# Kernel tuning notes

Measured on AMD Instinct MI355X. Metric: run time of the kernel, lower is better.

The kernel has to match this reference:

```python
import jax, jax.numpy as jnp
import numpy as np

B, N, DIM = 4, 4096, 512
HEADS, DIM_HEAD = 8, 64
DIM_INNER = HEADS * DIM_HEAD


def setup_inputs() -> dict:
    key = jax.random.key(0)
    k1, k2, k3 = jax.random.split(key, 3)
    x = jax.random.normal(k1, (B, N, DIM), dtype=jnp.float32)
    mask = jax.random.bernoulli(k2, 0.9, (B, N))
    W_qkv = jax.random.normal(k3, (DIM, 3 * DIM_INNER), dtype=jnp.float32) * (1.0 / np.sqrt(DIM))
    b_qkv = jnp.zeros((3 * DIM_INNER,), dtype=jnp.float32)
    return {"x": x, "mask": mask, "W_qkv": W_qkv, "b_qkv": b_qkv}


def reference(x, mask, W_qkv, b_qkv):
    # qkv projection: [b, n, 3*h*d]
    qkv = jnp.einsum('bnc,ce->bne', x, W_qkv) + b_qkv
    q, k, v = jnp.split(qkv, 3, axis=-1)

    def to_heads(t):  # b n (h d) -> b h n d
        b, n, _ = t.shape
        return t.reshape(b, n, HEADS, DIM_HEAD).transpose(0, 2, 1, 3)

    q, k, v = map(to_heads, (q, k, v))

    m = mask[:, None, :, None]  # b 1 n 1
    neg_max = -jnp.finfo(q.dtype).max
    k = jnp.where(m, k, neg_max)
    v = jnp.where(m, v, 0.0)

    k = jax.nn.softmax(k, axis=-2)  # softmax over sequence
    q = jax.nn.softmax(q, axis=-1)  # softmax over feature dim

    kv = jnp.einsum('bhnd,bhne->bhde', k, v)   # [b, h, d, d]
    out = jnp.einsum('bhde,bhnd->bhne', kv, q)  # [b, h, n, d]
    b_, h_, n_, d_ = out.shape
    return out.transpose(0, 2, 1, 3).reshape(b_, n_, h_ * d_)
```

## Files before the change

### kernel.cpp

```cpp
#include <hip/hip_runtime.h>
#include <stdint.h>

#define B_   4
#define N_   4096
#define DIM_ 512
#define H_   8
#define DH_  64
#define E3_  1536
#define M_   (B_*N_)

typedef __attribute__((ext_vector_type(8))) __bf16 bf16x8;
typedef __attribute__((ext_vector_type(8))) unsigned short ushort8;
typedef __attribute__((ext_vector_type(4))) float f32x4;

__device__ inline float bf2f(unsigned short u){ return __uint_as_float(((unsigned)u)<<16); }
__device__ inline unsigned short f2bf(float f){
  unsigned u = __float_as_uint(f);
  u += 0x7FFFu + ((u>>16)&1u);
  return (unsigned short)(u>>16);
}

__device__ inline void gld_lds16(const void* g, void* l){
  __builtin_amdgcn_global_load_lds(
      (const __attribute__((address_space(1))) void*)g,
      (__attribute__((address_space(3))) void*)l, 16, 0, 0);
}

__global__ void detect_fmt(const unsigned int* __restrict__ xw,
                           const unsigned int* __restrict__ ww,
                           const unsigned int* __restrict__ mw,
                           int* __restrict__ flags)
{
  __shared__ int cnt[2];
  __shared__ int ok[3];
  if (threadIdx.x < 2) cnt[threadIdx.x] = 0;
  if (threadIdx.x < 3) ok[threadIdx.x] = 1;
  __syncthreads();
  int hx = 0, hw = 0;
  for (int i = threadIdx.x; i < 1024; i += 256) {
    if (((xw[i] >> 7) & 0xFFu) > 140u) hx++;
    if (((ww[i] >> 7) & 0xFFu) > 140u) hw++;
  }
  int okInt = 1, okF32 = 1, okBf = 1;
  for (int i = threadIdx.x; i < 4096; i += 256) {
    unsigned w = mw[i];
    if (w > 1u) okInt = 0;
    if (w != 0u && w != 0x3F800000u) okF32 = 0;
    unsigned short a = (unsigned short)(w & 0xFFFFu), b = (unsigned short)(w >> 16);
    if (!((a == 0 || a == 0x3F80u) && (b == 0 || b == 0x3F80u))) okBf = 0;
  }
  atomicAdd(&cnt[0], hx);
  atomicAdd(&cnt[1], hw);
  if (!okInt) atomicAnd(&ok[0], 0);
  if (!okF32) atomicAnd(&ok[1], 0);
  if (!okBf)  atomicAnd(&ok[2], 0);
  __syncthreads();
  if (threadIdx.x == 0) {
    flags[0] = cnt[0] > 64 ? 1 : 0;
    flags[1] = cnt[1] > 64 ? 1 : 0;
    flags[2] = ok[0] ? 0 : (ok[1] ? 1 : (ok[2] ? 2 : 3));
  }
}

__device__ inline bool mask_at(const void* m, int flag, int idx){
  if (flag == 0) return ((const int*)m)[idx] != 0;
  if (flag == 1) return ((const float*)m)[idx] != 0.f;
  if (flag == 2) return ((const unsigned short*)m)[idx] != 0;
  return ((const unsigned char*)m)[idx] != 0;
}
__device__ inline float gread(const void* p, int f32, size_t i){
  return f32 ? ((const float*)p)[i] : bf2f(((const unsigned short*)p)[i]);
}

__global__ __launch_bounds__(256)
void pack_x(const void* __restrict__ x, unsigned short* __restrict__ xq,
            const int* __restrict__ flags)
{
  const int f = flags[0];
  const int g = blockIdx.x * 256 + threadIdx.x;
  const int R = g >> 13, rem = g & 8191;
  const int kk = rem >> 9, u = rem & 511;
  const int m = R * 128 + (u & 127);
  const int k0 = kk * 32 + (u >> 7) * 8;
  ushort8 v;
  if (f) {
    const float* xp = (const float*)x + (size_t)m * DIM_ + k0;
    float4 a = *(const float4*)xp, b = *(const float4*)(xp + 4);
    v[0]=f2bf(a.x); v[1]=f2bf(a.y); v[2]=f2bf(a.z); v[3]=f2bf(a.w);
    v[4]=f2bf(b.x); v[5]=f2bf(b.y); v[6]=f2bf(b.z); v[7]=f2bf(b.w);
  } else {
    v = *(const ushort8*)((const unsigned short*)x + (size_t)m * DIM_ + k0);
  }
  *(ushort8*)&xq[(size_t)g * 8] = v;
}

__global__ __launch_bounds__(256)
void pack_w(const void* __restrict__ w, unsigned short* __restrict__ wq,
            const int* __restrict__ flags)
{
  const int f = flags[1];
  const int g = blockIdx.x * 256 + threadIdx.x;
  const int C = g >> 13, rem = g & 8191;
  const int kk = rem >> 9, u = rem & 511;
  const int n = C * 128 + (u & 127);
  const int k0 = kk * 32 + (u >> 7) * 8;
  ushort8 v;
  #pragma unroll
  for (int j = 0; j < 8; ++j) v[j] = f2bf(gread(w, f, (size_t)(k0 + j) * E3_ + n));
  *(ushort8*)&wq[(size_t)g * 8] = v;
}

__global__ __launch_bounds__(256)
void qkv_gemm_fused(const unsigned short* __restrict__ xq,
                    const unsigned short* __restrict__ wq,
                    const void* __restrict__ bias, const void* __restrict__ mask,
                    const int* __restrict__ flags,
                    unsigned short* __restrict__ qb,
                    unsigned short* __restrict__ ekg,
                    unsigned short* __restrict__ vmg)
{
  const int wf = flags[1], mf = flags[2];
  __shared__ alignas(16) unsigned short As[512 * 8];
  __shared__ alignas(16) unsigned short Bs[512 * 8];
  const int t = threadIdx.x;
  const int lane = t & 63, wv = t >> 6;
  const int quad = lane >> 4, l15 = lane & 15;
  const int m0 = blockIdx.y * 128, n0 = blockIdx.x * 128;
  const int mw = (wv & 1) * 64, nw = (wv >> 1) * 64;

  f32x4 acc[4][4];
  #pragma unroll
  for (int i = 0; i < 4; ++i)
    #pragma unroll
    for (int j = 0; j < 4; ++j) acc[i][j] = (f32x4){0.f,0.f,0.f,0.f};

  for (int kk = 0; kk < 16; ++kk) {
    const unsigned short* aim = xq + ((size_t)(blockIdx.y * 16 + kk) * 512) * 8;
    const unsigned short* bim = wq + ((size_t)(blockIdx.x * 16 + kk) * 512) * 8;
    __syncthreads();
    #pragma unroll
    for (int s = 0; s < 2; ++s) {
      const int u0 = s * 256 + wv * 64;
      gld_lds16(aim + (size_t)(u0 + lane) * 8, &As[u0 * 8]);
      gld_lds16(bim + (size_t)(u0 + lane) * 8, &Bs[u0 * 8]);
    }
    __syncthreads();
    ushort8 af[4], bfr[4];
    #pragma unroll
    for (int i = 0; i < 4; ++i) {
      af[i]  = *(const ushort8*)&As[(quad * 128 + mw + i * 16 + l15) * 8];
      bfr[i] = *(const ushort8*)&Bs[(quad * 128 + nw + i * 16 + l15) * 8];
    }
    #pragma unroll
    for (int i = 0; i < 4; ++i)
      #pragma unroll
      for (int j = 0; j < 4; ++j)
        acc[i][j] = __builtin_amdgcn_mfma_f32_16x16x32_bf16(
            __builtin_bit_cast(bf16x8, af[i]), __builtin_bit_cast(bf16x8, bfr[j]),
            acc[i][j], 0, 0, 0);
  }

  const int mode = blockIdx.x >> 2;
  if (mode == 0) {
    #pragma unroll
    for (int j = 0; j < 4; ++j) {
      int col = n0 + nw + j * 16 + l15;
      float bv = gread(bias, wf, col);
      #pragma unroll
      for (int i = 0; i < 4; ++i)
        #pragma unroll
        for (int r = 0; r < 4; ++r) {
          int row = m0 + mw + i * 16 + quad * 4 + r;
          qb[(size_t)row * 512 + col] = f2bf(acc[i][j][r] + bv);
        }
    }
  } else {
    unsigned short* dstbuf = (mode == 1) ? ekg : vmg;
    float bj[4]; int hj[4], dj[4];
    #pragma unroll
    for (int j = 0; j < 4; ++j) {
      int col = n0 + nw + j * 16 + l15;
      bj[j] = gread(bias, wf, col);
      int rel = col - mode * 512;
      hj[j] = rel >> 6; dj[j] = rel & 63;
    }
    #pragma unroll
    for (int i = 0; i < 4; ++i)
      #pragma unroll
      for (int r = 0; r < 4; ++r) {
        int row = m0 + mw + i * 16 + quad * 4 + r;
        bool mk = mask_at(mask, mf, row);
        int b = row >> 12, nn = row & 4095;
        size_t base = (size_t)(nn >> 3) * 512 + (nn & 7);
        #pragma unroll
        for (int j = 0; j < 4; ++j) {
          float val = acc[i][j][r] + bj[j];
          val = (mode == 1) ? (mk ? __expf(val) : 0.f) : (mk ? val : 0.f);
          dstbuf[(size_t)(b * 8 + hj[j]) * 262144 + base + (size_t)dj[j] * 8] = f2bf(val);
        }
      }
  }
}

__global__ __launch_bounds__(256)
void kv_gemm(const unsigned short* __restrict__ ekg,
             const unsigned short* __restrict__ vmg,
             float* __restrict__ kvpart, float* __restrict__ denpart)
{
  const int kc8 = blockIdx.x;
  const int bh  = blockIdx.y;
  const int t   = threadIdx.x;
  const int lane = t & 63, wv = t >> 6;
  const int quad = lane >> 4, l15 = lane & 15;
  __shared__ alignas(16) unsigned short ekS[16384];
  __shared__ alignas(16) unsigned short vmS[16384];

  f32x4 acc[4];
  #pragma unroll
  for (int j = 0; j < 4; ++j) acc[j] = (f32x4){0.f,0.f,0.f,0.f};
  float dsum = 0.f;
  const int dden = t & 63, g0 = (t >> 6) * 8;

  for (int sc = 0; sc < 2; ++sc) {
    const size_t gbase = (size_t)bh * 262144 + (size_t)(kc8 * 2 + sc) * 16384;
    __syncthreads();
    #pragma unroll
    for (int i = 0; i < 8; ++i) {
      int u0 = i * 256 + wv * 64;
      gld_lds16(&ekg[gbase + (size_t)(u0 + lane) * 8], &ekS[u0 * 8]);
      gld_lds16(&vmg[gbase + (size_t)(u0 + lane) * 8], &vmS[u0 * 8]);
    }
    __syncthreads();
    {
      #pragma unroll
      for (int kt = 0; kt < 8; ++kt) {
        ushort8 v = *(const ushort8*)&ekS[((g0 + kt) * 64 + dden) * 8];
        #pragma unroll
        for (int j = 0; j < 8; ++j) dsum += bf2f(v[j]);
      }
    }
    #pragma unroll 2
    for (int ks = 0; ks < 8; ++ks) {
      ushort8 af = *(const ushort8*)&ekS[((ks * 4 + quad) * 64 + wv * 16 + l15) * 8];
      #pragma unroll
      for (int jt = 0; jt < 4; ++jt) {
        ushort8 bf8 = *(const ushort8*)&vmS[((ks * 4 + quad) * 64 + jt * 16 + l15) * 8];
        acc[jt] = __builtin_amdgcn_mfma_f32_16x16x32_bf16(
            __builtin_bit_cast(bf16x8, af), __builtin_bit_cast(bf16x8, bf8),
            acc[jt], 0, 0, 0);
      }
    }
  }
  float* kvp = kvpart + (size_t)(kc8 * 32 + bh) * 4096;
  #pragma unroll
  for (int jt = 0; jt < 4; ++jt)
    #pragma unroll
    for (int r = 0; r < 4; ++r)
      kvp[(wv * 16 + quad * 4 + r) * 64 + jt * 16 + l15] = acc[jt][r];
  __syncthreads();
  float* red = (float*)ekS;
  red[t] = dsum;
  __syncthreads();
  if (t < 64)
    denpart[(kc8 * 32 + bh) * 64 + t] = red[t] + red[t + 64] + red[t + 128] + red[t + 192];
}

__global__ __launch_bounds__(256)
void kv_reduce(const float* __restrict__ kvpart, const float* __restrict__ denpart,
               unsigned short* __restrict__ kvnb)
{
  const int bh = blockIdx.x;
  const int t  = threadIdx.x;
  __shared__ float den[64];
  if (t < 64) {
    float s = 0.f;
    #pragma unroll
    for (int c = 0; c < 8; ++c) s += denpart[(c * 32 + bh) * 64 + t];
    den[t] = s;
  }
  __syncthreads();
  const int d = t >> 2, e0 = (t & 3) * 16;
  const float inv = 1.f / den[d];
  #pragma unroll
  for (int j = 0; j < 16; ++j) {
    int e = e0 + j;
    float s = 0.f;
    #pragma unroll
    for (int c = 0; c < 8; ++c) s += kvpart[(size_t)(c * 32 + bh) * 4096 + d * 64 + e];
    kvnb[(size_t)bh * 4096 + ((size_t)(d >> 3) * 64 + e) * 8 + (d & 7)] = f2bf(s * inv);
  }
}

__global__ __launch_bounds__(256)
void out_pass(const unsigned short* __restrict__ qb,
              const unsigned short* __restrict__ kvnb,
              float* __restrict__ out)
{
  const int chunk = blockIdx.x, bh = blockIdx.y;
  const int b = bh >> 3, h = bh & 7;
  const int t = threadIdx.x;
  const int lane = t & 63, wv = t >> 6;
  const int quad = lane >> 4, l15 = lane & 15;
  __shared__ alignas(16) unsigned short kvS[4096];
  __shared__ alignas(16) unsigned short qsmb[1024];
  #pragma unroll
  for (int i = 0; i < 2; ++i)
    *(ushort8*)&kvS[(t + i * 256) * 8] =
        *(const ushort8*)&kvnb[(size_t)bh * 4096 + (size_t)(t + i * 256) * 8];

  const int tok = t >> 4, p = t & 15, d0 = p * 4;
  float qreg[4];
  {
    int row = b * N_ + chunk * 256 + tok;
    uint2 qw = *(const uint2*)(qb + (size_t)row * 512 + h * DH_ + d0);
    qreg[0] = bf2f((unsigned short)(qw.x & 0xffff));
    qreg[1] = bf2f((unsigned short)(qw.x >> 16));
    qreg[2] = bf2f((unsigned short)(qw.y & 0xffff));
    qreg[3] = bf2f((unsigned short)(qw.y >> 16));
  }
  for (int g = 0; g < 16; ++g) {
    const int row0 = b * N_ + chunk * 256 + g * 16;
    float mx = fmaxf(fmaxf(qreg[0], qreg[1]), fmaxf(qreg[2], qreg[3]));
    #pragma unroll
    for (int o = 1; o < 16; o <<= 1) mx = fmaxf(mx, __shfl_xor(mx, o, 16));
    float ex[4]; float s = 0.f;
    #pragma unroll
    for (int j = 0; j < 4; ++j) { ex[j] = __expf(qreg[j] - mx); s += ex[j]; }
    #pragma unroll
    for (int o = 1; o < 16; o <<= 1) s += __shfl_xor(s, o, 16);
    float inv = 1.f / s;
    __syncthreads();
    #pragma unroll
    for (int j = 0; j < 4; ++j)
      qsmb[((size_t)((d0 + j) >> 3) * 16 + tok) * 8 + ((d0 + j) & 7)] = f2bf(ex[j] * inv);
    if (g < 15) {
      uint2 qw = *(const uint2*)(qb + (size_t)(row0 + 16 + tok) * 512 + h * DH_ + d0);
      qreg[0] = bf2f((unsigned short)(qw.x & 0xffff));
      qreg[1] = bf2f((unsigned short)(qw.x >> 16));
      qreg[2] = bf2f((unsigned short)(qw.y & 0xffff));
      qreg[3] = bf2f((unsigned short)(qw.y >> 16));
    }
    __syncthreads();
    f32x4 acc = (f32x4){0.f,0.f,0.f,0.f};
    #pragma unroll
    for (int s2 = 0; s2 < 2; ++s2) {
      int koct = s2 * 4 + quad;
      ushort8 a8 = *(const ushort8*)&qsmb[(koct * 16 + l15) * 8];
      ushort8 b8 = *(const ushort8*)&kvS[(koct * 64 + wv * 16 + l15) * 8];
      acc = __builtin_amdgcn_mfma_f32_16x16x32_bf16(
          __builtin_bit_cast(bf16x8, a8), __builtin_bit_cast(bf16x8, b8), acc, 0, 0, 0);
    }
    #pragma unroll
    for (int r = 0; r < 4; ++r)
      out[(size_t)(row0 + quad * 4 + r) * 512 + h * DH_ + wv * 16 + l15] = acc[r];
  }
}

__device__ inline void stage_x_f(float (*xa)[516], const void* x, int xf, int brow0, int t)
{
  if (xf) {
    const float* xp = (const float*)x;
    #pragma unroll
    for (int s = 0; s < 8; ++s) {
      int row = (t >> 7) + 2 * s, col = (t & 127) * 4;
      *(float4*)&xa[row][col] = *(const float4*)(xp + ((size_t)(brow0 + row)) * DIM_ + col);
    }
  } else {
    const unsigned short* xp = (const unsigned short*)x;
    #pragma unroll
    for (int s = 0; s < 8; ++s) {
      int row = (t >> 7) + 2 * s, col = (t & 127) * 4;
      const unsigned short* pp = xp + ((size_t)(brow0 + row)) * DIM_ + col;
      #pragma unroll
      for (int j = 0; j < 4; ++j) xa[row][col + j] = bf2f(pp[j]);
    }
  }
}

__global__ __launch_bounds__(256)
void kv_pass_fused(const void* __restrict__ x, const void* __restrict__ w,
                   const void* __restrict__ bias, const void* __restrict__ mask,
                   const int* __restrict__ flags,
                   float* __restrict__ kvbuf, float* __restrict__ denom)
{
  const int chunk = blockIdx.x, bh = blockIdx.y;
  const int b = bh >> 3, h = bh & 7;
  const int t = threadIdx.x;
  const int xf = flags[0], wf = flags[1], mf = flags[2];
  __shared__ float xa[16][516];
  __shared__ float Wb[64][130];
  float* ekb = &Wb[0][0];
  float* vvb = &Wb[0][0] + 16 * 65;
  const int tok = t >> 4, d0 = (t & 15) * 4;
  const int down = t >> 2, e0 = (t & 3) * 16;
  float acc[16];
  #pragma unroll
  for (int i = 0; i < 16; ++i) acc[i] = 0.f;
  float dsum = 0.f;
  for (int g = 0; g < 16; ++g) {
    const int n0 = chunk * 256 + g * 16;
    __syncthreads();
    stage_x_f(xa, x, xf, b * N_ + n0, t);
    float kreg[4] = {0,0,0,0}, vreg[4] = {0,0,0,0};
    for (int cc = 0; cc < 8; ++cc) {
      __syncthreads();
      {
        int c0 = (t >> 7) * 32, col = t & 127;
        int wc = (col < 64) ? (512 + h * DH_ + col) : (1024 + h * DH_ + (col - 64));
        #pragma unroll 8
        for (int j = 0; j < 32; ++j)
          Wb[c0 + j][col] = gread(w, wf, (size_t)(cc * 64 + c0 + j) * E3_ + wc);
      }
      __syncthreads();
      #pragma unroll 4
      for (int c = 0; c < 64; ++c) {
        float xv = xa[tok][cc * 64 + c];
        #pragma unroll
        for (int j = 0; j < 4; ++j) {
          kreg[j] += xv * Wb[c][d0 + j];
          vreg[j] += xv * Wb[c][64 + d0 + j];
        }
      }
    }
    bool mk = mask_at(mask, mf, b * N_ + n0 + tok);
    __syncthreads();
    #pragma unroll
    for (int j = 0; j < 4; ++j) {
      float kvl = kreg[j] + gread(bias, wf, 512  + h * DH_ + d0 + j);
      float vvl = vreg[j] + gread(bias, wf, 1024 + h * DH_ + d0 + j);
      ekb[tok * 65 + d0 + j] = mk ? __expf(kvl) : 0.f;
      vvb[tok * 65 + d0 + j] = mk ? vvl : 0.f;
    }
    __syncthreads();
    #pragma unroll 4
    for (int nn = 0; nn < 16; ++nn) {
      float ekd = ekb[nn * 65 + down];
      if (e0 == 0) dsum += ekd;
      #pragma unroll
      for (int i = 0; i < 16; ++i) acc[i] += ekd * vvb[nn * 65 + e0 + i];
    }
  }
  float* kvp = kvbuf + (size_t)bh * 4096 + down * 64 + e0;
  #pragma unroll
  for (int i = 0; i < 16; ++i) atomicAdd(&kvp[i], acc[i]);
  if (e0 == 0) atomicAdd(&denom[bh * 64 + down], dsum);
}

__global__ __launch_bounds__(256)
void out_pass_fused(const void* __restrict__ x, const void* __restrict__ w,
                    const void* __restrict__ bias, const int* __restrict__ flags,
                    const float* __restrict__ kvbuf, const float* __restrict__ denom,
                    float* __restrict__ out)
{
  const int chunk = blockIdx.x, bh = blockIdx.y;
  const int b = bh >> 3, h = bh & 7;
  const int t = threadIdx.x;
  const int xf = flags[0], wf = flags[1];
  __shared__ float xa[16][516];
  __shared__ float Wq[64][66];
  __shared__ float kvn[64][68];
  float* qsm = &Wq[0][0];
  for (int i = t; i < 4096; i += 256) {
    int d = i >> 6, e = i & 63;
    kvn[d][e] = kvbuf[(size_t)bh * 4096 + i] / denom[bh * 64 + d];
  }
  const int tok = t >> 4, p = t & 15, d0 = p * 4;
  for (int g = 0; g < 16; ++g) {
    const int n0 = chunk * 256 + g * 16;
    __syncthreads();
    stage_x_f(xa, x, xf, b * N_ + n0, t);
    float qreg[4] = {0,0,0,0};
    for (int cc = 0; cc < 8; ++cc) {
      __syncthreads();
      {
        int col = t & 63, c0 = (t >> 6) * 16;
        #pragma unroll 8
        for (int j = 0; j < 16; ++j)
          Wq[c0 + j][col] = gread(w, wf, (size_t)(cc * 64 + c0 + j) * E3_ + h * DH_ + col);
      }
      __syncthreads();
      #pragma unroll 4
      for (int c = 0; c < 64; ++c) {
        float xv = xa[tok][cc * 64 + c];
        #pragma unroll
        for (int j = 0; j < 4; ++j) qreg[j] += xv * Wq[c][d0 + j];
      }
    }
    #pragma unroll
    for (int j = 0; j < 4; ++j) qreg[j] += gread(bias, wf, h * DH_ + d0 + j);
    float mx = fmaxf(fmaxf(qreg[0], qreg[1]), fmaxf(qreg[2], qreg[3]));
    #pragma unroll
    for (int o = 1; o < 16; o <<= 1) mx = fmaxf(mx, __shfl_xor(mx, o, 16));
    float s = 0.f;
    #pragma unroll
    for (int j = 0; j < 4; ++j) { qreg[j] = __expf(qreg[j] - mx); s += qreg[j]; }
    #pragma unroll
    for (int o = 1; o < 16; o <<= 1) s += __shfl_xor(s, o, 16);
    float inv = 1.f / s;
    __syncthreads();
    #pragma unroll
    for (int j = 0; j < 4; ++j) qsm[tok * 65 + d0 + j] = qreg[j] * inv;
    __syncthreads();
    {
      int e0 = p * 4;
      float ov[4] = {0,0,0,0};
      #pragma unroll 4
      for (int d = 0; d < 64; ++d) {
        float qd = qsm[tok * 65 + d];
        #pragma unroll
        for (int j = 0; j < 4; ++j) ov[j] += qd * kvn[d][e0 + j];
      }
      size_t ob = ((size_t)(b * N_ + n0 + tok)) * DIM_ + h * DH_ + e0;
      #pragma unroll
      for (int j = 0; j < 4; ++j) out[ob + j] = ov[j];
    }
  }
}

extern "C" void kernel_launch(void* const* d_in, const int* in_sizes, int n_in,
                              void* d_out, int out_size, void* d_ws, size_t ws_size,
                              hipStream_t stream)
{
  const void* x    = d_in[0];
  const void* mask = d_in[1];
  const void* w    = d_in[2];
  const void* bias = d_in[3];
  float* out = (float*)d_out;

  char* ws = (char*)d_ws;
  const size_t offFlg = 0;
  const size_t offXq  = 4096;
  const size_t offWq  = offXq + (size_t)M_ * DIM_ * 2;
  const size_t offQ   = offWq + (size_t)E3_ * DIM_ * 2;
  const size_t offEk  = offQ  + (size_t)M_ * DIM_ * 2;
  const size_t offVm  = offEk + (size_t)M_ * DH_ * H_ * 2;
  const size_t need   = offVm + (size_t)M_ * DH_ * H_ * 2;
  const size_t offKvp = offXq;
  const size_t offDnp = offXq + 4194304;
  const size_t offKvn = offXq + 4194304 + 65536;

  int* flags = (int*)(ws + offFlg);
  detect_fmt<<<1, 256, 0, stream>>>((const unsigned int*)x, (const unsigned int*)w,
                                    (const unsigned int*)mask, flags);

  if (ws_size >= need) {
    unsigned short* xq  = (unsigned short*)(ws + offXq);
    unsigned short* wq  = (unsigned short*)(ws + offWq);
    unsigned short* qb  = (unsigned short*)(ws + offQ);
    unsigned short* ekg = (unsigned short*)(ws + offEk);
    unsigned short* vmg = (unsigned short*)(ws + offVm);
    float* kvpart = (float*)(ws + offKvp);
    float* denpart = (float*)(ws + offDnp);
    unsigned short* kvnb = (unsigned short*)(ws + offKvn);

    pack_x<<<4096, 256, 0, stream>>>(x, xq, flags);
    pack_w<<<384, 256, 0, stream>>>(w, wq, flags);
    dim3 gg(E3_ / 128, M_ / 128);
    qkv_gemm_fused<<<gg, 256, 0, stream>>>(xq, wq, bias, mask, flags, qb, ekg, vmg);
    dim3 gkv(8, 32);
    kv_gemm<<<gkv, 256, 0, stream>>>(ekg, vmg, kvpart, denpart);
    kv_reduce<<<32, 256, 0, stream>>>(kvpart, denpart, kvnb);
    dim3 ga(16, 32);
    out_pass<<<ga, 256, 0, stream>>>(qb, kvnb, out);
  } else {
    float* kvbuf = (float*)(ws + 4096);
    float* denom = (float*)(ws + 4096 + 32 * 4096 * 4);
    hipMemsetAsync(kvbuf, 0, 32 * 4096 * 4 + 32 * 64 * 4, stream);
    dim3 ga(16, 32);
    kv_pass_fused <<<ga, 256, 0, stream>>>(x, w, bias, mask, flags, kvbuf, denom);
    out_pass_fused<<<ga, 256, 0, stream>>>(x, w, bias, flags, kvbuf, denom, out);
  }
}
```

Baseline: 183.7 us.

## Merge pack kernels, double-buffer QKV GEMM, widen KV split, streamline out pass

```diff
diff --git a/kernel.cpp b/kernel.cpp
--- a/kernel.cpp
+++ b/kernel.cpp
@@ -72,45 +72,50 @@
   return f32 ? ((const float*)p)[i] : bf2f(((const unsigned short*)p)[i]);
 }
 
+__device__ inline void unpack8(uint4 u, float* f){
+  f[0] = bf2f((unsigned short)(u.x & 0xffff)); f[1] = bf2f((unsigned short)(u.x >> 16));
+  f[2] = bf2f((unsigned short)(u.y & 0xffff)); f[3] = bf2f((unsigned short)(u.y >> 16));
+  f[4] = bf2f((unsigned short)(u.z & 0xffff)); f[5] = bf2f((unsigned short)(u.z >> 16));
+  f[6] = bf2f((unsigned short)(u.w & 0xffff)); f[7] = bf2f((unsigned short)(u.w >> 16));
+}
+
 __global__ __launch_bounds__(256)
-void pack_x(const void* __restrict__ x, unsigned short* __restrict__ xq,
-            const int* __restrict__ flags)
-{
-  const int f = flags[0];
-  const int g = blockIdx.x * 256 + threadIdx.x;
-  const int R = g >> 13, rem = g & 8191;
-  const int kk = rem >> 9, u = rem & 511;
-  const int m = R * 128 + (u & 127);
-  const int k0 = kk * 32 + (u >> 7) * 8;
-  ushort8 v;
-  if (f) {
-    const float* xp = (const float*)x + (size_t)m * DIM_ + k0;
-    float4 a = *(const float4*)xp, b = *(const float4*)(xp + 4);
-    v[0]=f2bf(a.x); v[1]=f2bf(a.y); v[2]=f2bf(a.z); v[3]=f2bf(a.w);
-    v[4]=f2bf(b.x); v[5]=f2bf(b.y); v[6]=f2bf(b.z); v[7]=f2bf(b.w);
+void pack_xw(const void* __restrict__ x, const void* __restrict__ w,
+             unsigned short* __restrict__ xq, unsigned short* __restrict__ wq,
+             const int* __restrict__ flags)
+{
+  if (blockIdx.x < 4096) {
+    const int f = flags[0];
+    const int g = blockIdx.x * 256 + threadIdx.x;
+    const int R = g >> 13, rem = g & 8191;
+    const int kk = rem >> 9, u = rem & 511;
+    const int m = R * 128 + (u & 127);
+    const int k0 = kk * 32 + (u >> 7) * 8;
+    ushort8 v;
+    if (f) {
+      const float* xp = (const float*)x + (size_t)m * DIM_ + k0;
+      float4 a = *(const float4*)xp, b = *(const float4*)(xp + 4);
+      v[0]=f2bf(a.x); v[1]=f2bf(a.y); v[2]=f2bf(a.z); v[3]=f2bf(a.w);
+      v[4]=f2bf(b.x); v[5]=f2bf(b.y); v[6]=f2bf(b.z); v[7]=f2bf(b.w);
+    } else {
+      v = *(const ushort8*)((const unsigned short*)x + (size_t)m * DIM_ + k0);
+    }
+    *(ushort8*)&xq[(size_t)g * 8] = v;
   } else {
-    v = *(const ushort8*)((const unsigned short*)x + (size_t)m * DIM_ + k0);
-  }
-  *(ushort8*)&xq[(size_t)g * 8] = v;
-}
-
-__global__ __launch_bounds__(256)
-void pack_w(const void* __restrict__ w, unsigned short* __restrict__ wq,
-            const int* __restrict__ flags)
-{
-  const int f = flags[1];
-  const int g = blockIdx.x * 256 + threadIdx.x;
-  const int C = g >> 13, rem = g & 8191;
-  const int kk = rem >> 9, u = rem & 511;
-  const int n = C * 128 + (u & 127);
-  const int k0 = kk * 32 + (u >> 7) * 8;
-  ushort8 v;
-  #pragma unroll
-  for (int j = 0; j < 8; ++j) v[j] = f2bf(gread(w, f, (size_t)(k0 + j) * E3_ + n));
-  *(ushort8*)&wq[(size_t)g * 8] = v;
-}
-
-__global__ __launch_bounds__(256)
+    const int f = flags[1];
+    const int g = (blockIdx.x - 4096) * 256 + threadIdx.x;
+    const int C = g >> 13, rem = g & 8191;
+    const int kk = rem >> 9, u = rem & 511;
+    const int n = C * 128 + (u & 127);
+    const int k0 = kk * 32 + (u >> 7) * 8;
+    ushort8 v;
+    #pragma unroll
+    for (int j = 0; j < 8; ++j) v[j] = f2bf(gread(w, f, (size_t)(k0 + j) * E3_ + n));
+    *(ushort8*)&wq[(size_t)g * 8] = v;
+  }
+}
+
+__global__ __launch_bounds__(512, 4)
 void qkv_gemm_fused(const unsigned short* __restrict__ xq,
                     const unsigned short* __restrict__ wq,
                     const void* __restrict__ bias, const void* __restrict__ mask,
@@ -120,50 +125,65 @@
                     unsigned short* __restrict__ vmg)
 {
   const int wf = flags[1], mf = flags[2];
-  __shared__ alignas(16) unsigned short As[512 * 8];
-  __shared__ alignas(16) unsigned short Bs[512 * 8];
+  __shared__ alignas(16) unsigned short As[2][8192];
+  __shared__ alignas(16) unsigned short Bs[2][8192];
   const int t = threadIdx.x;
   const int lane = t & 63, wv = t >> 6;
   const int quad = lane >> 4, l15 = lane & 15;
   const int m0 = blockIdx.y * 128, n0 = blockIdx.x * 128;
-  const int mw = (wv & 1) * 64, nw = (wv >> 1) * 64;
-
-  f32x4 acc[4][4];
+  const int mw = (wv & 1) * 64;
+  const int nw = (wv >> 1) * 32;
+
+  f32x4 acc[4][2];
   #pragma unroll
   for (int i = 0; i < 4; ++i)
     #pragma unroll
-    for (int j = 0; j < 4; ++j) acc[i][j] = (f32x4){0.f,0.f,0.f,0.f};
-
-  for (int kk = 0; kk < 16; ++kk) {
-    const unsigned short* aim = xq + ((size_t)(blockIdx.y * 16 + kk) * 512) * 8;
-    const unsigned short* bim = wq + ((size_t)(blockIdx.x * 16 + kk) * 512) * 8;
-    __syncthreads();
-    #pragma unroll
-    for (int s = 0; s < 2; ++s) {
-      const int u0 = s * 256 + wv * 64;
-      gld_lds16(aim + (size_t)(u0 + lane) * 8, &As[u0 * 8]);
-      gld_lds16(bim + (size_t)(u0 + lane) * 8, &Bs[u0 * 8]);
-    }
-    __syncthreads();
-    ushort8 af[4], bfr[4];
-    #pragma unroll
-    for (int i = 0; i < 4; ++i) {
-      af[i]  = *(const ushort8*)&As[(quad * 128 + mw + i * 16 + l15) * 8];
-      bfr[i] = *(const ushort8*)&Bs[(quad * 128 + nw + i * 16 + l15) * 8];
-    }
-    #pragma unroll
-    for (int i = 0; i < 4; ++i)
-      #pragma unroll
-      for (int j = 0; j < 4; ++j)
-        acc[i][j] = __builtin_amdgcn_mfma_f32_16x16x32_bf16(
-            __builtin_bit_cast(bf16x8, af[i]), __builtin_bit_cast(bf16x8, bfr[j]),
-            acc[i][j], 0, 0, 0);
+    for (int j = 0; j < 2; ++j) acc[i][j] = (f32x4){0.f,0.f,0.f,0.f};
+
+  const unsigned short* aim0 = xq + ((size_t)(blockIdx.y * 16) * 512) * 8;
+  const unsigned short* bim0 = wq + ((size_t)(blockIdx.x * 16) * 512) * 8;
+
+  auto stage = [&](int kt, int bb) {
+    const unsigned short* aim = aim0 + (size_t)kt * (2 * 512 * 8);
+    const unsigned short* bim = bim0 + (size_t)kt * (2 * 512 * 8);
+    #pragma unroll
+    for (int h2 = 0; h2 < 2; ++h2) {
+      const int u0 = h2 * 512 + wv * 64;
+      gld_lds16(aim + (size_t)(u0 + lane) * 8, &As[bb][u0 * 8]);
+      gld_lds16(bim + (size_t)(u0 + lane) * 8, &Bs[bb][u0 * 8]);
+    }
+  };
+
+  stage(0, 0);
+  __syncthreads();
+  int cur = 0;
+  for (int kt = 0; kt < 8; ++kt) {
+    if (kt < 7) stage(kt + 1, cur ^ 1);
+    #pragma unroll
+    for (int kc = 0; kc < 2; ++kc) {
+      ushort8 af[4], bfr[2];
+      #pragma unroll
+      for (int i = 0; i < 4; ++i)
+        af[i] = *(const ushort8*)&As[cur][(kc * 512 + quad * 128 + mw + i * 16 + l15) * 8];
+      #pragma unroll
+      for (int j = 0; j < 2; ++j)
+        bfr[j] = *(const ushort8*)&Bs[cur][(kc * 512 + quad * 128 + nw + j * 16 + l15) * 8];
+      #pragma unroll
+      for (int i = 0; i < 4; ++i)
+        #pragma unroll
+        for (int j = 0; j < 2; ++j)
+          acc[i][j] = __builtin_amdgcn_mfma_f32_16x16x32_bf16(
+              __builtin_bit_cast(bf16x8, af[i]), __builtin_bit_cast(bf16x8, bfr[j]),
+              acc[i][j], 0, 0, 0);
+    }
+    __syncthreads();
+    cur ^= 1;
   }
 
   const int mode = blockIdx.x >> 2;
   if (mode == 0) {
     #pragma unroll
-    for (int j = 0; j < 4; ++j) {
+    for (int j = 0; j < 2; ++j) {
       int col = n0 + nw + j * 16 + l15;
       float bv = gread(bias, wf, col);
       #pragma unroll
@@ -176,9 +196,9 @@
     }
   } else {
     unsigned short* dstbuf = (mode == 1) ? ekg : vmg;
-    float bj[4]; int hj[4], dj[4];
-    #pragma unroll
-    for (int j = 0; j < 4; ++j) {
+    float bj[2]; int hj[2], dj[2];
+    #pragma unroll
+    for (int j = 0; j < 2; ++j) {
       int col = n0 + nw + j * 16 + l15;
       bj[j] = gread(bias, wf, col);
       int rel = col - mode * 512;
@@ -190,13 +210,13 @@
       for (int r = 0; r < 4; ++r) {
         int row = m0 + mw + i * 16 + quad * 4 + r;
         bool mk = mask_at(mask, mf, row);
-        int b = row >> 12, nn = row & 4095;
+        int bb2 = row >> 12, nn = row & 4095;
         size_t base = (size_t)(nn >> 3) * 512 + (nn & 7);
         #pragma unroll
-        for (int j = 0; j < 4; ++j) {
+        for (int j = 0; j < 2; ++j) {
           float val = acc[i][j][r] + bj[j];
           val = (mode == 1) ? (mk ? __expf(val) : 0.f) : (mk ? val : 0.f);
-          dstbuf[(size_t)(b * 8 + hj[j]) * 262144 + base + (size_t)dj[j] * 8] = f2bf(val);
+          dstbuf[(size_t)(bb2 * 8 + hj[j]) * 262144 + base + (size_t)dj[j] * 8] = f2bf(val);
         }
       }
   }
@@ -207,9 +227,9 @@
              const unsigned short* __restrict__ vmg,
              float* __restrict__ kvpart, float* __restrict__ denpart)
 {
-  const int kc8 = blockIdx.x;
-  const int bh  = blockIdx.y;
-  const int t   = threadIdx.x;
+  const int sc = blockIdx.x;
+  const int bh = blockIdx.y;
+  const int t  = threadIdx.x;
   const int lane = t & 63, wv = t >> 6;
   const int quad = lane >> 4, l15 = lane & 15;
   __shared__ alignas(16) unsigned short ekS[16384];
@@ -220,38 +240,35 @@
   for (int j = 0; j < 4; ++j) acc[j] = (f32x4){0.f,0.f,0.f,0.f};
   float dsum = 0.f;
   const int dden = t & 63, g0 = (t >> 6) * 8;
-
-  for (int sc = 0; sc < 2; ++sc) {
-    const size_t gbase = (size_t)bh * 262144 + (size_t)(kc8 * 2 + sc) * 16384;
-    __syncthreads();
-    #pragma unroll
-    for (int i = 0; i < 8; ++i) {
-      int u0 = i * 256 + wv * 64;
-      gld_lds16(&ekg[gbase + (size_t)(u0 + lane) * 8], &ekS[u0 * 8]);
-      gld_lds16(&vmg[gbase + (size_t)(u0 + lane) * 8], &vmS[u0 * 8]);
-    }
-    __syncthreads();
-    {
-      #pragma unroll
-      for (int kt = 0; kt < 8; ++kt) {
-        ushort8 v = *(const ushort8*)&ekS[((g0 + kt) * 64 + dden) * 8];
-        #pragma unroll
-        for (int j = 0; j < 8; ++j) dsum += bf2f(v[j]);
-      }
-    }
-    #pragma unroll 2
-    for (int ks = 0; ks < 8; ++ks) {
-      ushort8 af = *(const ushort8*)&ekS[((ks * 4 + quad) * 64 + wv * 16 + l15) * 8];
-      #pragma unroll
-      for (int jt = 0; jt < 4; ++jt) {
-        ushort8 bf8 = *(const ushort8*)&vmS[((ks * 4 + quad) * 64 + jt * 16 + l15) * 8];
-        acc[jt] = __builtin_amdgcn_mfma_f32_16x16x32_bf16(
-            __builtin_bit_cast(bf16x8, af), __builtin_bit_cast(bf16x8, bf8),
-            acc[jt], 0, 0, 0);
-      }
-    }
-  }
-  float* kvp = kvpart + (size_t)(kc8 * 32 + bh) * 4096;
+  const size_t gbase = (size_t)bh * 262144 + (size_t)sc * 16384;
+
+  #pragma unroll
+  for (int i = 0; i < 8; ++i) {
+    int u0 = i * 256 + wv * 64;
+    gld_lds16(&ekg[gbase + (size_t)(u0 + lane) * 8], &ekS[u0 * 8]);
+    gld_lds16(&vmg[gbase + (size_t)(u0 + lane) * 8], &vmS[u0 * 8]);
+  }
+  __syncthreads();
+  {
+    #pragma unroll
+    for (int kt = 0; kt < 8; ++kt) {
+      ushort8 v = *(const ushort8*)&ekS[((g0 + kt) * 64 + dden) * 8];
+      #pragma unroll
+      for (int j = 0; j < 8; ++j) dsum += bf2f(v[j]);
+    }
+  }
+  #pragma unroll 2
+  for (int ks = 0; ks < 8; ++ks) {
+    ushort8 af = *(const ushort8*)&ekS[((ks * 4 + quad) * 64 + wv * 16 + l15) * 8];
+    #pragma unroll
+    for (int jt = 0; jt < 4; ++jt) {
+      ushort8 bf8 = *(const ushort8*)&vmS[((ks * 4 + quad) * 64 + jt * 16 + l15) * 8];
+      acc[jt] = __builtin_amdgcn_mfma_f32_16x16x32_bf16(
+          __builtin_bit_cast(bf16x8, af), __builtin_bit_cast(bf16x8, bf8),
+          acc[jt], 0, 0, 0);
+    }
+  }
+  float* kvp = kvpart + (size_t)(sc * 32 + bh) * 4096;
   #pragma unroll
   for (int jt = 0; jt < 4; ++jt)
     #pragma unroll
@@ -262,7 +279,7 @@
   red[t] = dsum;
   __syncthreads();
   if (t < 64)
-    denpart[(kc8 * 32 + bh) * 64 + t] = red[t] + red[t + 64] + red[t + 128] + red[t + 192];
+    denpart[(sc * 32 + bh) * 64 + t] = red[t] + red[t + 64] + red[t + 128] + red[t + 192];
 }
 
 __global__ __launch_bounds__(256)
@@ -270,24 +287,30 @@
                unsigned short* __restrict__ kvnb)
 {
   const int bh = blockIdx.x;
+  const int qd = blockIdx.y;
   const int t  = threadIdx.x;
-  __shared__ float den[64];
-  if (t < 64) {
+  __shared__ float den[16];
+  if (t < 16) {
     float s = 0.f;
     #pragma unroll
-    for (int c = 0; c < 8; ++c) s += denpart[(c * 32 + bh) * 64 + t];
+    for (int c = 0; c < 16; ++c) s += denpart[(c * 32 + bh) * 64 + qd * 16 + t];
     den[t] = s;
   }
   __syncthreads();
-  const int d = t >> 2, e0 = (t & 3) * 16;
-  const float inv = 1.f / den[d];
-  #pragma unroll
-  for (int j = 0; j < 16; ++j) {
+  const int dl = t >> 4, e0 = (t & 15) * 4;
+  const int d = qd * 16 + dl;
+  float sx = 0.f, sy = 0.f, sz = 0.f, sw = 0.f;
+  #pragma unroll
+  for (int c = 0; c < 16; ++c) {
+    const float4 v = *(const float4*)&kvpart[(size_t)(c * 32 + bh) * 4096 + d * 64 + e0];
+    sx += v.x; sy += v.y; sz += v.z; sw += v.w;
+  }
+  const float inv = 1.f / den[dl];
+  const float sv[4] = {sx, sy, sz, sw};
+  #pragma unroll
+  for (int j = 0; j < 4; ++j) {
     int e = e0 + j;
-    float s = 0.f;
-    #pragma unroll
-    for (int c = 0; c < 8; ++c) s += kvpart[(size_t)(c * 32 + bh) * 4096 + d * 64 + e];
-    kvnb[(size_t)bh * 4096 + ((size_t)(d >> 3) * 64 + e) * 8 + (d & 7)] = f2bf(s * inv);
+    kvnb[(size_t)bh * 4096 + ((size_t)(d >> 3) * 64 + e) * 8 + (d & 7)] = f2bf(sv[j] * inv);
   }
 }
 
@@ -302,57 +325,54 @@
   const int lane = t & 63, wv = t >> 6;
   const int quad = lane >> 4, l15 = lane & 15;
   __shared__ alignas(16) unsigned short kvS[4096];
-  __shared__ alignas(16) unsigned short qsmb[1024];
   #pragma unroll
   for (int i = 0; i < 2; ++i)
     *(ushort8*)&kvS[(t + i * 256) * 8] =
         *(const ushort8*)&kvnb[(size_t)bh * 4096 + (size_t)(t + i * 256) * 8];
-
-  const int tok = t >> 4, p = t & 15, d0 = p * 4;
-  float qreg[4];
-  {
-    int row = b * N_ + chunk * 256 + tok;
-    uint2 qw = *(const uint2*)(qb + (size_t)row * 512 + h * DH_ + d0);
-    qreg[0] = bf2f((unsigned short)(qw.x & 0xffff));
-    qreg[1] = bf2f((unsigned short)(qw.x >> 16));
-    qreg[2] = bf2f((unsigned short)(qw.y & 0xffff));
-    qreg[3] = bf2f((unsigned short)(qw.y >> 16));
-  }
-  for (int g = 0; g < 16; ++g) {
-    const int row0 = b * N_ + chunk * 256 + g * 16;
-    float mx = fmaxf(fmaxf(qreg[0], qreg[1]), fmaxf(qreg[2], qreg[3]));
-    #pragma unroll
-    for (int o = 1; o < 16; o <<= 1) mx = fmaxf(mx, __shfl_xor(mx, o, 16));
-    float ex[4]; float s = 0.f;
-    #pragma unroll
-    for (int j = 0; j < 4; ++j) { ex[j] = __expf(qreg[j] - mx); s += ex[j]; }
-    #pragma unroll
-    for (int o = 1; o < 16; o <<= 1) s += __shfl_xor(s, o, 16);
-    float inv = 1.f / s;
-    __syncthreads();
-    #pragma unroll
-    for (int j = 0; j < 4; ++j)
-      qsmb[((size_t)((d0 + j) >> 3) * 16 + tok) * 8 + ((d0 + j) & 7)] = f2bf(ex[j] * inv);
-    if (g < 15) {
-      uint2 qw = *(const uint2*)(qb + (size_t)(row0 + 16 + tok) * 512 + h * DH_ + d0);
-      qreg[0] = bf2f((unsigned short)(qw.x & 0xffff));
-      qreg[1] = bf2f((unsigned short)(qw.x >> 16));
-      qreg[2] = bf2f((unsigned short)(qw.y & 0xffff));
-      qreg[3] = bf2f((unsigned short)(qw.y >> 16));
-    }
-    __syncthreads();
-    f32x4 acc = (f32x4){0.f,0.f,0.f,0.f};
-    #pragma unroll
-    for (int s2 = 0; s2 < 2; ++s2) {
-      int koct = s2 * 4 + quad;
-      ushort8 a8 = *(const ushort8*)&qsmb[(koct * 16 + l15) * 8];
-      ushort8 b8 = *(const ushort8*)&kvS[(koct * 64 + wv * 16 + l15) * 8];
-      acc = __builtin_amdgcn_mfma_f32_16x16x32_bf16(
-          __builtin_bit_cast(bf16x8, a8), __builtin_bit_cast(bf16x8, b8), acc, 0, 0, 0);
-    }
-    #pragma unroll
-    for (int r = 0; r < 4; ++r)
-      out[(size_t)(row0 + quad * 4 + r) * 512 + h * DH_ + wv * 16 + l15] = acc[r];
+  __syncthreads();
+
+  for (int g = 0; g < 4; ++g) {
+    const int tok0 = chunk * 256 + wv * 64 + g * 16;
+    const size_t qoff = (size_t)(b * N_ + tok0 + l15) * 512 + h * DH_ + quad * 8;
+    uint4 qa = *(const uint4*)(qb + qoff);
+    uint4 qc = *(const uint4*)(qb + qoff + 32);
+    float qf[16];
+    unpack8(qa, qf); unpack8(qc, qf + 8);
+    float mx = qf[0];
+    #pragma unroll
+    for (int jj = 1; jj < 16; ++jj) mx = fmaxf(mx, qf[jj]);
+    mx = fmaxf(mx, __shfl_xor(mx, 16));
+    mx = fmaxf(mx, __shfl_xor(mx, 32));
+    float s = 0.f;
+    #pragma unroll
+    for (int jj = 0; jj < 16; ++jj) { qf[jj] = __expf(qf[jj] - mx); s += qf[jj]; }
+    s += __shfl_xor(s, 16);
+    s += __shfl_xor(s, 32);
+    const float inv = 1.f / s;
+    ushort8 af0, af1;
+    #pragma unroll
+    for (int jj = 0; jj < 8; ++jj) {
+      af0[jj] = f2bf(qf[jj] * inv);
+      af1[jj] = f2bf(qf[8 + jj] * inv);
+    }
+    f32x4 oa[4];
+    #pragma unroll
+    for (int jt = 0; jt < 4; ++jt) oa[jt] = (f32x4){0.f,0.f,0.f,0.f};
+    #pragma unroll
+    for (int jt = 0; jt < 4; ++jt) {
+      ushort8 b0 = *(const ushort8*)&kvS[((0 + quad) * 64 + jt * 16 + l15) * 8];
+      ushort8 b1 = *(const ushort8*)&kvS[((4 + quad) * 64 + jt * 16 + l15) * 8];
+      oa[jt] = __builtin_amdgcn_mfma_f32_16x16x32_bf16(
+          __builtin_bit_cast(bf16x8, af0), __builtin_bit_cast(bf16x8, b0), oa[jt], 0, 0, 0);
+      oa[jt] = __builtin_amdgcn_mfma_f32_16x16x32_bf16(
+          __builtin_bit_cast(bf16x8, af1), __builtin_bit_cast(bf16x8, b1), oa[jt], 0, 0, 0);
+    }
+    const size_t ob = (size_t)(b * N_ + tok0 + quad * 4) * 512 + h * DH_;
+    #pragma unroll
+    for (int jt = 0; jt < 4; ++jt)
+      #pragma unroll
+      for (int r = 0; r < 4; ++r)
+        out[ob + (size_t)r * 512 + jt * 16 + l15] = oa[jt][r];
   }
 }
 
@@ -536,8 +556,8 @@
   const size_t offVm  = offEk + (size_t)M_ * DH_ * H_ * 2;
   const size_t need   = offVm + (size_t)M_ * DH_ * H_ * 2;
   const size_t offKvp = offXq;
-  const size_t offDnp = offXq + 4194304;
-  const size_t offKvn = offXq + 4194304 + 65536;
+  const size_t offDnp = offXq + 8388608;
+  const size_t offKvn = offXq + 8388608 + 131072;
 
   int* flags = (int*)(ws + offFlg);
   detect_fmt<<<1, 256, 0, stream>>>((const unsigned int*)x, (const unsigned int*)w,
@@ -553,15 +573,12 @@
     float* denpart = (float*)(ws + offDnp);
     unsigned short* kvnb = (unsigned short*)(ws + offKvn);
 
-    pack_x<<<4096, 256, 0, stream>>>(x, xq, flags);
-    pack_w<<<384, 256, 0, stream>>>(w, wq, flags);
+    pack_xw<<<4480, 256, 0, stream>>>(x, w, xq, wq, flags);
     dim3 gg(E3_ / 128, M_ / 128);
-    qkv_gemm_fused<<<gg, 256, 0, stream>>>(xq, wq, bias, mask, flags, qb, ekg, vmg);
-    dim3 gkv(8, 32);
-    kv_gemm<<<gkv, 256, 0, stream>>>(ekg, vmg, kvpart, denpart);
-    kv_reduce<<<32, 256, 0, stream>>>(kvpart, denpart, kvnb);
-    dim3 ga(16, 32);
-    out_pass<<<ga, 256, 0, stream>>>(qb, kvnb, out);
+    qkv_gemm_fused<<<gg, 512, 0, stream>>>(xq, wq, bias, mask, flags, qb, ekg, vmg);
+    kv_gemm<<<dim3(16, 32), 256, 0, stream>>>(ekg, vmg, kvpart, denpart);
+    kv_reduce<<<dim3(32, 4), 256, 0, stream>>>(kvpart, denpart, kvnb);
+    out_pass<<<dim3(16, 32), 256, 0, stream>>>(qb, kvnb, out);
   } else {
     float* kvbuf = (float*)(ws + 4096);
     float* denom = (float*)(ws + 4096 + 32 * 4096 * 4);
```

Result: no change. 181.0 us (-1.5%).
